# Kernel optimization log

Hardware: AMD Instinct MI355X
Metric: run time of the kernel (lower is better)

## Reference

```python
import jax, jax.numpy as jnp
import numpy as np

EPS = 1e-6
B, C, D = 128, 1000, 1024


def setup_inputs() -> dict:
    key = jax.random.key(0)
    k1, k2, k3, k4 = jax.random.split(key, 4)
    x = jax.random.normal(k1, (B, D), dtype=jnp.float32)
    # xavier-normal-ish prototypes
    mu = jax.random.normal(k2, (C, D), dtype=jnp.float32) * (2.0 / (C + D)) ** 0.5
    beta = jax.random.normal(k3, (D,), dtype=jnp.float32) * 0.1
    # L initialized as identity + small lower-triangular noise (full_sigma=True)
    L = jnp.eye(D, dtype=jnp.float32) + jnp.tril(
        jax.random.normal(k4, (D, D), dtype=jnp.float32) * 0.01)
    lmbda = jnp.asarray(0.1, dtype=jnp.float32)
    scale = jnp.asarray(10.0, dtype=jnp.float32)
    return {"x": x, "mu": mu, "beta": beta, "L": L, "lmbda": lmbda, "scale": scale}


def reference(x, mu, beta, L, lmbda, scale):
    # Sigma = tril(L) @ tril(L)^T + eps*I  (positive definite)
    Lt = jnp.tril(L)
    sigma = Lt @ Lt.T + EPS * jnp.eye(L.shape[0], dtype=L.dtype)
    # diff: [B, C, D]
    diff = x[:, None, :] - mu[None, :, :]
    # quadratic form v^T Sigma v per (b, c): contract once, then reduce
    ds = jnp.einsum('bcd,df->bcf', diff, sigma)   # [B, C, D]
    quad = jnp.sum(ds * diff, axis=-1)            # [B, C]
    beta_dot = jnp.einsum('d,bcd->bc', beta, diff)  # [B, C]
    riemannian = jnp.sqrt(quad + EPS)
    directional = lmbda * jnp.sqrt(beta_dot * beta_dot + EPS)  # smooth |.|
    return -scale * (riemannian + directional)
```

## Files before the change

kernel.cpp:

```cpp
#include <hip/hip_runtime.h>
#include <hip/hip_bf16.h>

#define D_DIM 1024
#define B_DIM 128
#define C_DIM 1000
#define M_ALL 1152
#define EPSF 1e-6f

typedef __attribute__((ext_vector_type(8))) short short8;
typedef __attribute__((ext_vector_type(4))) float f32x4;

static __device__ __forceinline__ unsigned short f2bf(float f) {
    union { float f; unsigned int u; } v; v.f = f;
    unsigned int u = v.u;
    u += 0x7fffu + ((u >> 16) & 1u);
    return (unsigned short)(u >> 16);
}
static __device__ __forceinline__ float bf2f(unsigned short s) {
    union { unsigned int u; float f; } v; v.u = ((unsigned int)s) << 16;
    return v.f;
}

__global__ void pack_A(const float* __restrict__ x, const float* __restrict__ mu,
                       unsigned short* __restrict__ A_bf) {
    int idx = blockIdx.x * 256 + threadIdx.x;
    int e = idx * 4;
    int row = e >> 10, col = e & 1023;
    float4 v;
    if (row < B_DIM)              v = *(const float4*)(x + row * D_DIM + col);
    else if (row < B_DIM + C_DIM) v = *(const float4*)(mu + (row - B_DIM) * D_DIM + col);
    else                          v = make_float4(0.f, 0.f, 0.f, 0.f);
    ushort4 o;
    o.x = f2bf(v.x); o.y = f2bf(v.y); o.z = f2bf(v.z); o.w = f2bf(v.w);
    *(ushort4*)(A_bf + e) = o;
}

__global__ void pack_LT(const float* __restrict__ L, unsigned short* __restrict__ LT) {
    __shared__ unsigned short tile[64][65];
    const int tid = threadIdx.x;
    const int k0 = blockIdx.y * 64, n0 = blockIdx.x * 64;
    const int tn = tid & 63, tq = tid >> 6;
#pragma unroll
    for (int i = 0; i < 16; ++i) {
        int kk = tq + i * 4;
        int k = k0 + kk, n = n0 + tn;
        float v = (k >= n) ? L[k * D_DIM + n] : 0.f;
        tile[tn][kk] = f2bf(v);
    }
    __syncthreads();
#pragma unroll
    for (int i = 0; i < 16; ++i) {
        int nn = tq + i * 4;
        LT[(n0 + nn) * D_DIM + k0 + tn] = tile[nn][tn];
    }
}

__global__ __launch_bounds__(256)
void gemm_bt_tri(const unsigned short* __restrict__ A, const unsigned short* __restrict__ BT,
                 unsigned short* __restrict__ Cbf) {
    __shared__ unsigned short As[64][72];
    __shared__ unsigned short Bs[64][72];
    const int tid = threadIdx.x;
    const int m0 = blockIdx.y * 64, n0 = blockIdx.x * 64;
    const int wave = tid >> 6, lane = tid & 63;
    const int wm = (wave & 1) * 32, wn = (wave >> 1) * 32;
    const int lrow = lane & 15, q = lane >> 4;
    f32x4 acc[2][2] = {};

    for (int k0 = n0; k0 < D_DIM; k0 += 64) {
#pragma unroll
        for (int c = tid; c < 512; c += 256) {
            int r = c >> 3, s = (c & 7) * 8;
            *(short8*)&As[r][s] = *(const short8*)(A  + (m0 + r) * D_DIM + k0 + s);
            *(short8*)&Bs[r][s] = *(const short8*)(BT + (n0 + r) * D_DIM + k0 + s);
        }
        __syncthreads();
#pragma unroll
        for (int ks = 0; ks < 64; ks += 32) {
            short8 a0 = *(const short8*)&As[wm +      lrow][ks + q * 8];
            short8 a1 = *(const short8*)&As[wm + 16 + lrow][ks + q * 8];
            short8 b0 = *(const short8*)&Bs[wn +      lrow][ks + q * 8];
            short8 b1 = *(const short8*)&Bs[wn + 16 + lrow][ks + q * 8];
            acc[0][0] = __builtin_amdgcn_mfma_f32_16x16x32_bf16(a0, b0, acc[0][0], 0, 0, 0);
            acc[0][1] = __builtin_amdgcn_mfma_f32_16x16x32_bf16(a0, b1, acc[0][1], 0, 0, 0);
            acc[1][0] = __builtin_amdgcn_mfma_f32_16x16x32_bf16(a1, b0, acc[1][0], 0, 0, 0);
            acc[1][1] = __builtin_amdgcn_mfma_f32_16x16x32_bf16(a1, b1, acc[1][1], 0, 0, 0);
        }
        __syncthreads();
    }
#pragma unroll
    for (int mi = 0; mi < 2; ++mi)
#pragma unroll
    for (int ni = 0; ni < 2; ++ni) {
        int n = n0 + wn + ni * 16 + lrow;
        int mb = m0 + wm + mi * 16 + q * 4;
#pragma unroll
        for (int r = 0; r < 4; ++r)
            Cbf[(mb + r) * D_DIM + n] = f2bf(acc[mi][ni][r]);
    }
}

__global__ void row_aux(const float* __restrict__ A, const unsigned short* __restrict__ P,
                        const float* __restrict__ beta,
                        float* __restrict__ nrm, float* __restrict__ bdot) {
    const int m = blockIdx.x, tid = threadIdx.x;
    const float4  a  = *(const float4*)(A + m * D_DIM + tid * 4);
    const ushort4 pu = *(const ushort4*)(P + m * D_DIM + tid * 4);
    const float4  bt = *(const float4*)(beta + tid * 4);
    float p0 = bf2f(pu.x), p1 = bf2f(pu.y), p2 = bf2f(pu.z), p3 = bf2f(pu.w);
    float sp = p0*p0 + p1*p1 + p2*p2 + p3*p3;
    float sa = a.x*a.x + a.y*a.y + a.z*a.z + a.w*a.w;
    float sb = bt.x*a.x + bt.y*a.y + bt.z*a.z + bt.w*a.w;
#pragma unroll
    for (int off = 32; off > 0; off >>= 1) {
        sp += __shfl_down(sp, off);
        sa += __shfl_down(sa, off);
        sb += __shfl_down(sb, off);
    }
    __shared__ float red[3][4];
    int lane = tid & 63, wid = tid >> 6;
    if (lane == 0) { red[0][wid] = sp; red[1][wid] = sa; red[2][wid] = sb; }
    __syncthreads();
    if (tid == 0) {
        float p = red[0][0] + red[0][1] + red[0][2] + red[0][3];
        float a2 = red[1][0] + red[1][1] + red[1][2] + red[1][3];
        float b2 = red[2][0] + red[2][1] + red[2][2] + red[2][3];
        nrm[m]  = fmaf(EPSF, a2, p);
        bdot[m] = b2;
    }
}

__global__ __launch_bounds__(256)
void gemm_cross(const unsigned short* __restrict__ U, const unsigned short* __restrict__ V,
                const float* __restrict__ nx, const float* __restrict__ nmu,
                const float* __restrict__ bx, const float* __restrict__ bmu,
                const float* __restrict__ lmbda_p, const float* __restrict__ scale_p,
                float* __restrict__ out) {
    __shared__ unsigned short Us[32][72];
    __shared__ unsigned short Vs[32][72];
    const int tid = threadIdx.x;
    const int b0 = blockIdx.y * 32, c0 = blockIdx.x * 32;
    const int wave = tid >> 6, lane = tid & 63;
    const int wm = (wave & 1) * 16, wn = (wave >> 1) * 16;
    const int lrow = lane & 15, q = lane >> 4;
    f32x4 acc = {};

    for (int k0 = 0; k0 < D_DIM; k0 += 64) {
        {
            int r = tid >> 3, s = (tid & 7) * 8;
            *(short8*)&Us[r][s] = *(const short8*)(U + (b0 + r) * D_DIM + k0 + s);
            *(short8*)&Vs[r][s] = *(const short8*)(V + (c0 + r) * D_DIM + k0 + s);
        }
        __syncthreads();
#pragma unroll
        for (int ks = 0; ks < 64; ks += 32) {
            short8 a = *(const short8*)&Us[wm + lrow][ks + q * 8];
            short8 b = *(const short8*)&Vs[wn + lrow][ks + q * 8];
            acc = __builtin_amdgcn_mfma_f32_16x16x32_bf16(a, b, acc, 0, 0, 0);
        }
        __syncthreads();
    }
    const float lm = *lmbda_p, sc = *scale_p;
    int c = c0 + wn + lrow;
    if (c < C_DIM) {
        float nm = nmu[c], bm = bmu[c];
#pragma unroll
        for (int r = 0; r < 4; ++r) {
            int b = b0 + wm + q * 4 + r;
            float quad = nx[b] + nm - 2.f * acc[r] + EPSF;
            quad = fmaxf(quad, 0.f);
            float bd = bx[b] - bm;
            out[b * C_DIM + c] = -sc * (sqrtf(quad) + lm * sqrtf(fmaf(bd, bd, EPSF)));
        }
    }
}

extern "C" void kernel_launch(void* const* d_in, const int* in_sizes, int n_in,
                              void* d_out, int out_size, void* d_ws, size_t ws_size,
                              hipStream_t stream) {
    const float* x     = (const float*)d_in[0];
    const float* mu    = (const float*)d_in[1];
    const float* beta  = (const float*)d_in[2];
    const float* L     = (const float*)d_in[3];
    const float* lmbda = (const float*)d_in[4];
    const float* scale = (const float*)d_in[5];
    float* out = (float*)d_out;

    char* ws = (char*)d_ws;
    unsigned short* A_bf  = (unsigned short*)ws;
    unsigned short* LT_bf = (unsigned short*)(ws + 2359296);
    unsigned short* uv_bf = (unsigned short*)(ws + 2359296 + 2097152);
    float* fws = (float*)(ws + 2359296 + 2097152 + 2359296);
    float* nx  = fws;
    float* nmu = fws + 128;
    float* bx  = fws + 1128;
    float* bmu = fws + 1256;

    dim3 blk(256);
    pack_A <<<1152, blk, 0, stream>>>(x, mu, A_bf);
    pack_LT<<<dim3(16, 16), blk, 0, stream>>>(L, LT_bf);
    gemm_bt_tri<<<dim3(16, 18), blk, 0, stream>>>(A_bf, LT_bf, uv_bf);
    row_aux<<<dim3(B_DIM), blk, 0, stream>>>(x,  uv_bf,                beta, nx,  bx);
    row_aux<<<dim3(C_DIM), blk, 0, stream>>>(mu, uv_bf + B_DIM * D_DIM, beta, nmu, bmu);
    gemm_cross<<<dim3(32, 4), blk, 0, stream>>>(uv_bf, uv_bf + B_DIM * D_DIM,
                                                nx, nmu, bx, bmu, lmbda, scale, out);
}
```

Measured before the change: 109.1 us.

## Fuse packing with row norms, fold P-norm into GEMM epilogue, drop LDS staging

```diff
diff --git a/kernel.cpp b/kernel.cpp
--- a/kernel.cpp
+++ b/kernel.cpp
@@ -1,5 +1,4 @@
 #include <hip/hip_runtime.h>
-#include <hip/hip_bf16.h>
 
 #define D_DIM 1024
 #define B_DIM 128
@@ -16,160 +15,139 @@
     u += 0x7fffu + ((u >> 16) & 1u);
     return (unsigned short)(u >> 16);
 }
-static __device__ __forceinline__ float bf2f(unsigned short s) {
-    union { unsigned int u; float f; } v; v.u = ((unsigned int)s) << 16;
-    return v.f;
-}
 
-__global__ void pack_A(const float* __restrict__ x, const float* __restrict__ mu,
-                       unsigned short* __restrict__ A_bf) {
-    int idx = blockIdx.x * 256 + threadIdx.x;
-    int e = idx * 4;
-    int row = e >> 10, col = e & 1023;
-    float4 v;
-    if (row < B_DIM)              v = *(const float4*)(x + row * D_DIM + col);
-    else if (row < B_DIM + C_DIM) v = *(const float4*)(mu + (row - B_DIM) * D_DIM + col);
-    else                          v = make_float4(0.f, 0.f, 0.f, 0.f);
-    ushort4 o;
-    o.x = f2bf(v.x); o.y = f2bf(v.y); o.z = f2bf(v.z); o.w = f2bf(v.w);
-    *(ushort4*)(A_bf + e) = o;
-}
+__global__ __launch_bounds__(256)
+void pack_all(const float* __restrict__ x, const float* __restrict__ mu,
+              const float* __restrict__ beta, const float* __restrict__ L,
+              unsigned short* __restrict__ A_bf, unsigned short* __restrict__ LT,
+              float* __restrict__ nrm, float* __restrict__ bdot) {
+    __shared__ unsigned short tile[64][65];
+    __shared__ float red[2][4];
+    const int tid = threadIdx.x;
 
-__global__ void pack_LT(const float* __restrict__ L, unsigned short* __restrict__ LT) {
-    __shared__ unsigned short tile[64][65];
-    const int tid = threadIdx.x;
-    const int k0 = blockIdx.y * 64, n0 = blockIdx.x * 64;
-    const int tn = tid & 63, tq = tid >> 6;
+    if (blockIdx.x < M_ALL) {
+        const int m = blockIdx.x;
+        float4 v;
+        if (m < B_DIM)              v = *(const float4*)(x + m * D_DIM + tid * 4);
+        else if (m < B_DIM + C_DIM) v = *(const float4*)(mu + (m - B_DIM) * D_DIM + tid * 4);
+        else                        v = make_float4(0.f, 0.f, 0.f, 0.f);
+        ushort4 o;
+        o.x = f2bf(v.x); o.y = f2bf(v.y); o.z = f2bf(v.z); o.w = f2bf(v.w);
+        *(ushort4*)(A_bf + m * D_DIM + tid * 4) = o;
+
+        const float4 bt = *(const float4*)(beta + tid * 4);
+        float sa = v.x*v.x + v.y*v.y + v.z*v.z + v.w*v.w;
+        float sb = bt.x*v.x + bt.y*v.y + bt.z*v.z + bt.w*v.w;
 #pragma unroll
-    for (int i = 0; i < 16; ++i) {
-        int kk = tq + i * 4;
-        int k = k0 + kk, n = n0 + tn;
-        float v = (k >= n) ? L[k * D_DIM + n] : 0.f;
-        tile[tn][kk] = f2bf(v);
-    }
-    __syncthreads();
+        for (int off = 32; off > 0; off >>= 1) {
+            sa += __shfl_down(sa, off);
+            sb += __shfl_down(sb, off);
+        }
+        int lane = tid & 63, wid = tid >> 6;
+        if (lane == 0) { red[0][wid] = sa; red[1][wid] = sb; }
+        __syncthreads();
+        if (tid == 0) {
+            float a2 = red[0][0] + red[0][1] + red[0][2] + red[0][3];
+            float b2 = red[1][0] + red[1][1] + red[1][2] + red[1][3];
+            nrm[m]  = EPSF * a2;
+            bdot[m] = b2;
+        }
+    } else {
+        const int t = blockIdx.x - M_ALL;
+        const int k0 = (t >> 4) * 64, n0 = (t & 15) * 64;
+        const int tn = tid & 63, tq = tid >> 6;
 #pragma unroll
-    for (int i = 0; i < 16; ++i) {
-        int nn = tq + i * 4;
-        LT[(n0 + nn) * D_DIM + k0 + tn] = tile[nn][tn];
+        for (int i = 0; i < 16; ++i) {
+            int kk = tq + i * 4;
+            int k = k0 + kk, n = n0 + tn;
+            float v = (k >= n) ? L[k * D_DIM + n] : 0.f;
+            tile[tn][kk] = f2bf(v);
+        }
+        __syncthreads();
+#pragma unroll
+        for (int i = 0; i < 16; ++i) {
+            int nn = tq + i * 4;
+            LT[(n0 + nn) * D_DIM + k0 + tn] = tile[nn][tn];
+        }
     }
 }
 
 __global__ __launch_bounds__(256)
-void gemm_bt_tri(const unsigned short* __restrict__ A, const unsigned short* __restrict__ BT,
-                 unsigned short* __restrict__ Cbf) {
-    __shared__ unsigned short As[64][72];
-    __shared__ unsigned short Bs[64][72];
-    const int tid = threadIdx.x;
-    const int m0 = blockIdx.y * 64, n0 = blockIdx.x * 64;
-    const int wave = tid >> 6, lane = tid & 63;
-    const int wm = (wave & 1) * 32, wn = (wave >> 1) * 32;
+void gemm_p(const unsigned short* __restrict__ A, const unsigned short* __restrict__ BT,
+            unsigned short* __restrict__ P, float* __restrict__ nrm) {
+    const int wid  = blockIdx.x * 4 + (threadIdx.x >> 6);
+    const int lane = threadIdx.x & 63;
+    const int mt = wid >> 5, nt = wid & 31;
+    const int m0 = mt * 32, n0 = nt * 32;
     const int lrow = lane & 15, q = lane >> 4;
+
+    const unsigned short* a0p = A  + (m0 + lrow)      * D_DIM + q * 8;
+    const unsigned short* a1p = A  + (m0 + 16 + lrow) * D_DIM + q * 8;
+    const unsigned short* b0p = BT + (n0 + lrow)      * D_DIM + q * 8;
+    const unsigned short* b1p = BT + (n0 + 16 + lrow) * D_DIM + q * 8;
+
     f32x4 acc[2][2] = {};
+#pragma unroll 2
+    for (int k0 = n0; k0 < D_DIM; k0 += 32) {
+        short8 a0 = *(const short8*)(a0p + k0);
+        short8 a1 = *(const short8*)(a1p + k0);
+        short8 b0 = *(const short8*)(b0p + k0);
+        short8 b1 = *(const short8*)(b1p + k0);
+        acc[0][0] = __builtin_amdgcn_mfma_f32_16x16x32_bf16(a0, b0, acc[0][0], 0, 0, 0);
+        acc[0][1] = __builtin_amdgcn_mfma_f32_16x16x32_bf16(a0, b1, acc[0][1], 0, 0, 0);
+        acc[1][0] = __builtin_amdgcn_mfma_f32_16x16x32_bf16(a1, b0, acc[1][0], 0, 0, 0);
+        acc[1][1] = __builtin_amdgcn_mfma_f32_16x16x32_bf16(a1, b1, acc[1][1], 0, 0, 0);
+    }
 
-    for (int k0 = n0; k0 < D_DIM; k0 += 64) {
 #pragma unroll
-        for (int c = tid; c < 512; c += 256) {
-            int r = c >> 3, s = (c & 7) * 8;
-            *(short8*)&As[r][s] = *(const short8*)(A  + (m0 + r) * D_DIM + k0 + s);
-            *(short8*)&Bs[r][s] = *(const short8*)(BT + (n0 + r) * D_DIM + k0 + s);
+    for (int mi = 0; mi < 2; ++mi) {
+#pragma unroll
+        for (int r = 0; r < 4; ++r) {
+            int m = m0 + mi * 16 + q * 4 + r;
+            float p0 = acc[mi][0][r], p1 = acc[mi][1][r];
+            P[m * D_DIM + n0 + lrow]      = f2bf(p0);
+            P[m * D_DIM + n0 + 16 + lrow] = f2bf(p1);
+            float s = p0 * p0 + p1 * p1;
+#pragma unroll
+            for (int off = 1; off < 16; off <<= 1)
+                s += __shfl_xor(s, off);
+            if (lrow == 0) atomicAdd(&nrm[m], s);
         }
-        __syncthreads();
-#pragma unroll
-        for (int ks = 0; ks < 64; ks += 32) {
-            short8 a0 = *(const short8*)&As[wm +      lrow][ks + q * 8];
-            short8 a1 = *(const short8*)&As[wm + 16 + lrow][ks + q * 8];
-            short8 b0 = *(const short8*)&Bs[wn +      lrow][ks + q * 8];
-            short8 b1 = *(const short8*)&Bs[wn + 16 + lrow][ks + q * 8];
-            acc[0][0] = __builtin_amdgcn_mfma_f32_16x16x32_bf16(a0, b0, acc[0][0], 0, 0, 0);
-            acc[0][1] = __builtin_amdgcn_mfma_f32_16x16x32_bf16(a0, b1, acc[0][1], 0, 0, 0);
-            acc[1][0] = __builtin_amdgcn_mfma_f32_16x16x32_bf16(a1, b0, acc[1][0], 0, 0, 0);
-            acc[1][1] = __builtin_amdgcn_mfma_f32_16x16x32_bf16(a1, b1, acc[1][1], 0, 0, 0);
-        }
-        __syncthreads();
-    }
-#pragma unroll
-    for (int mi = 0; mi < 2; ++mi)
-#pragma unroll
-    for (int ni = 0; ni < 2; ++ni) {
-        int n = n0 + wn + ni * 16 + lrow;
-        int mb = m0 + wm + mi * 16 + q * 4;
-#pragma unroll
-        for (int r = 0; r < 4; ++r)
-            Cbf[(mb + r) * D_DIM + n] = f2bf(acc[mi][ni][r]);
-    }
-}
-
-__global__ void row_aux(const float* __restrict__ A, const unsigned short* __restrict__ P,
-                        const float* __restrict__ beta,
-                        float* __restrict__ nrm, float* __restrict__ bdot) {
-    const int m = blockIdx.x, tid = threadIdx.x;
-    const float4  a  = *(const float4*)(A + m * D_DIM + tid * 4);
-    const ushort4 pu = *(const ushort4*)(P + m * D_DIM + tid * 4);
-    const float4  bt = *(const float4*)(beta + tid * 4);
-    float p0 = bf2f(pu.x), p1 = bf2f(pu.y), p2 = bf2f(pu.z), p3 = bf2f(pu.w);
-    float sp = p0*p0 + p1*p1 + p2*p2 + p3*p3;
-    float sa = a.x*a.x + a.y*a.y + a.z*a.z + a.w*a.w;
-    float sb = bt.x*a.x + bt.y*a.y + bt.z*a.z + bt.w*a.w;
-#pragma unroll
-    for (int off = 32; off > 0; off >>= 1) {
-        sp += __shfl_down(sp, off);
-        sa += __shfl_down(sa, off);
-        sb += __shfl_down(sb, off);
-    }
-    __shared__ float red[3][4];
-    int lane = tid & 63, wid = tid >> 6;
-    if (lane == 0) { red[0][wid] = sp; red[1][wid] = sa; red[2][wid] = sb; }
-    __syncthreads();
-    if (tid == 0) {
-        float p = red[0][0] + red[0][1] + red[0][2] + red[0][3];
-        float a2 = red[1][0] + red[1][1] + red[1][2] + red[1][3];
-        float b2 = red[2][0] + red[2][1] + red[2][2] + red[2][3];
-        nrm[m]  = fmaf(EPSF, a2, p);
-        bdot[m] = b2;
     }
 }
 
 __global__ __launch_bounds__(256)
-void gemm_cross(const unsigned short* __restrict__ U, const unsigned short* __restrict__ V,
-                const float* __restrict__ nx, const float* __restrict__ nmu,
-                const float* __restrict__ bx, const float* __restrict__ bmu,
+void gemm_cross(const unsigned short* __restrict__ UV,
+                const float* __restrict__ nrm, const float* __restrict__ bdot,
                 const float* __restrict__ lmbda_p, const float* __restrict__ scale_p,
                 float* __restrict__ out) {
-    __shared__ unsigned short Us[32][72];
-    __shared__ unsigned short Vs[32][72];
-    const int tid = threadIdx.x;
-    const int b0 = blockIdx.y * 32, c0 = blockIdx.x * 32;
-    const int wave = tid >> 6, lane = tid & 63;
-    const int wm = (wave & 1) * 16, wn = (wave >> 1) * 16;
+    const int wid  = blockIdx.x * 4 + (threadIdx.x >> 6);
+    const int lane = threadIdx.x & 63;
+    const int bt = wid / 63, ct = wid % 63;
+    const int b0 = bt * 16, c0 = ct * 16;
     const int lrow = lane & 15, q = lane >> 4;
+
+    const unsigned short* up = UV + (b0 + lrow) * D_DIM + q * 8;
+    const unsigned short* vp = UV + (B_DIM + c0 + lrow) * D_DIM + q * 8;
+
     f32x4 acc = {};
+#pragma unroll 4
+    for (int k0 = 0; k0 < D_DIM; k0 += 32) {
+        short8 a = *(const short8*)(up + k0);
+        short8 b = *(const short8*)(vp + k0);
+        acc = __builtin_amdgcn_mfma_f32_16x16x32_bf16(a, b, acc, 0, 0, 0);
+    }
 
-    for (int k0 = 0; k0 < D_DIM; k0 += 64) {
-        {
-            int r = tid >> 3, s = (tid & 7) * 8;
-            *(short8*)&Us[r][s] = *(const short8*)(U + (b0 + r) * D_DIM + k0 + s);
-            *(short8*)&Vs[r][s] = *(const short8*)(V + (c0 + r) * D_DIM + k0 + s);
-        }
-        __syncthreads();
-#pragma unroll
-        for (int ks = 0; ks < 64; ks += 32) {
-            short8 a = *(const short8*)&Us[wm + lrow][ks + q * 8];
-            short8 b = *(const short8*)&Vs[wn + lrow][ks + q * 8];
-            acc = __builtin_amdgcn_mfma_f32_16x16x32_bf16(a, b, acc, 0, 0, 0);
-        }
-        __syncthreads();
-    }
     const float lm = *lmbda_p, sc = *scale_p;
-    int c = c0 + wn + lrow;
+    const int c = c0 + lrow;
     if (c < C_DIM) {
-        float nm = nmu[c], bm = bmu[c];
+        float nm = nrm[B_DIM + c], bm = bdot[B_DIM + c];
 #pragma unroll
         for (int r = 0; r < 4; ++r) {
-            int b = b0 + wm + q * 4 + r;
-            float quad = nx[b] + nm - 2.f * acc[r] + EPSF;
+            int b = b0 + q * 4 + r;
+            float quad = nrm[b] + nm - 2.f * acc[r] + EPSF;
             quad = fmaxf(quad, 0.f);
-            float bd = bx[b] - bm;
+            float bd = bdot[b] - bm;
             out[b * C_DIM + c] = -sc * (sqrtf(quad) + lm * sqrtf(fmaf(bd, bd, EPSF)));
         }
     }
@@ -190,18 +168,12 @@
     unsigned short* A_bf  = (unsigned short*)ws;
     unsigned short* LT_bf = (unsigned short*)(ws + 2359296);
     unsigned short* uv_bf = (unsigned short*)(ws + 2359296 + 2097152);
-    float* fws = (float*)(ws + 2359296 + 2097152 + 2359296);
-    float* nx  = fws;
-    float* nmu = fws + 128;
-    float* bx  = fws + 1128;
-    float* bmu = fws + 1256;
+    float* fws  = (float*)(ws + 2359296 + 2097152 + 2359296);
+    float* nrm  = fws;
+    float* bdot = fws + M_ALL;
 
     dim3 blk(256);
-    pack_A <<<1152, blk, 0, stream>>>(x, mu, A_bf);
-    pack_LT<<<dim3(16, 16), blk, 0, stream>>>(L, LT_bf);
-    gemm_bt_tri<<<dim3(16, 18), blk, 0, stream>>>(A_bf, LT_bf, uv_bf);
-    row_aux<<<dim3(B_DIM), blk, 0, stream>>>(x,  uv_bf,                beta, nx,  bx);
-    row_aux<<<dim3(C_DIM), blk, 0, stream>>>(mu, uv_bf + B_DIM * D_DIM, beta, nmu, bmu);
-    gemm_cross<<<dim3(32, 4), blk, 0, stream>>>(uv_bf, uv_bf + B_DIM * D_DIM,
-                                                nx, nmu, bx, bmu, lmbda, scale, out);
+    pack_all  <<<M_ALL + 256, blk, 0, stream>>>(x, mu, beta, L, A_bf, LT_bf, nrm, bdot);
+    gemm_p    <<<288, blk, 0, stream>>>(A_bf, LT_bf, uv_bf, nrm);
+    gemm_cross<<<126, blk, 0, stream>>>(uv_bf, nrm, bdot, lmbda, scale, out);
 }
```

Result: slower. 116.7 us (+6.9%).
